# Optimization experiments

Measured on AMD Instinct MI355X. Metric: run time of the kernel, lower is better.

The kernel has to match this reference:

```python
import jax, jax.numpy as jnp
import numpy as np

B = 131072
D = 64          # d_model
T = 4           # num_tiles
TEMP = 0.5


def setup_inputs() -> dict:
    key = jax.random.key(0)
    ks = jax.random.split(key, 16)
    s = 0.02
    return {
        "a_vec": jax.random.normal(ks[0], (B, D), dtype=jnp.float32),
        "b_vec": jax.random.normal(ks[1], (B, D), dtype=jnp.float32),
        "pos_encoding": jax.random.normal(ks[2], (B, 8), dtype=jnp.float32),
        # router: Linear(2D+8 -> D), GELU, Linear(D -> T)
        "Wr1": jax.random.normal(ks[3], (2 * D + 8, D), dtype=jnp.float32) * s,
        "br1": jnp.zeros((D,), dtype=jnp.float32),
        "Wr2": jax.random.normal(ks[4], (D, T), dtype=jnp.float32) * s,
        "br2": jnp.zeros((T,), dtype=jnp.float32),
        # tile nets: per-tile Linear(2D -> 2D), GELU, Linear(2D -> D)
        "W1": jax.random.normal(ks[5], (T, 2 * D, 2 * D), dtype=jnp.float32) * s,
        "b1": jnp.zeros((T, 2 * D), dtype=jnp.float32),
        "W2": jax.random.normal(ks[6], (T, 2 * D, D), dtype=jnp.float32) * s,
        "b2": jnp.zeros((T, D), dtype=jnp.float32),
    }


def _router(x, Wr1, br1, Wr2, br2):
    h = jax.nn.gelu(x @ Wr1 + br1, approximate=False)  # torch nn.GELU is exact
    return (h @ Wr2 + br2) / TEMP


def reference(a_vec, b_vec, pos_encoding, Wr1, br1, Wr2, br2, W1, b1, W2, b2):
    pair = jnp.concatenate([a_vec, b_vec], axis=-1)            # (B, 2D)

    # Routing 1 uses pair; routing 2 uses flipped pair. Both expert passes
    # consume `pair` (faithful to the original code, which feeds pair both times).
    idx1 = jnp.argmax(_router(jnp.concatenate([pair, pos_encoding], -1),
                              Wr1, br1, Wr2, br2), axis=-1)    # (B,)
    pair_flip = jnp.concatenate([b_vec, a_vec], axis=-1)
    idx2 = jnp.argmax(_router(jnp.concatenate([pair_flip, pos_encoding], -1),
                              Wr1, br1, Wr2, br2), axis=-1)    # (B,)

    # Run all tiles on every sample (small T), then gather the routed output.
    h = jax.nn.gelu(jnp.einsum('bi,tij->btj', pair, W1) + b1, approximate=False)  # (B,T,2D)
    out_all = jnp.einsum('bth,thd->btd', h, W2) + b2                              # (B,T,D)

    out1 = jnp.take_along_axis(out_all, idx1[:, None, None], axis=1)[:, 0]
    out2 = jnp.take_along_axis(out_all, idx2[:, None, None], axis=1)[:, 0]
    return out1, out2
```

## Files before the change

kernel.cpp:

```cpp
#include <hip/hip_runtime.h>

#define B_N 131072

using bfrag_t = __attribute__((ext_vector_type(8))) short;
using acc_t   = __attribute__((ext_vector_type(4))) float;
using v4f     = __attribute__((ext_vector_type(4))) float;
using i32x4_t = __attribute__((ext_vector_type(4))) int;

__device__ __forceinline__ unsigned short f2bf(float f) {
  unsigned int u = __float_as_uint(f);
  u += 0x7FFFu + ((u >> 16) & 1u);
  return (unsigned short)(u >> 16);
}

__device__ __forceinline__ unsigned int pk2bf(float x, float y) {
  return (unsigned int)f2bf(x) | ((unsigned int)f2bf(y) << 16);
}

__device__ __forceinline__ void gload_lds16(const void* g, void* l) {
  __builtin_amdgcn_global_load_lds((const __attribute__((address_space(1))) void*)g,
                                   (__attribute__((address_space(3))) void*)l, 16, 0, 0);
}

__device__ __forceinline__ float gelu_f(float x) {
  float ax = fabsf(x) * 0.70710678118654752f;
  float t  = __builtin_amdgcn_rcpf(fmaf(0.3275911f, ax, 1.0f));
  float p  = fmaf(1.061405429f, t, -1.453152027f);
  p = fmaf(p, t, 1.421413741f);
  p = fmaf(p, t, -0.284496736f);
  p = fmaf(p, t, 0.254829592f);
  p = p * t;
  float e  = __expf(-ax * ax);
  float er = fmaf(-p, e, 1.0f);
  er = (x < 0.0f) ? -er : er;
  return 0.5f * x * (1.0f + er);
}

__global__ __launch_bounds__(256) void prepack2_k(
    const float* __restrict__ Wr1, const float* __restrict__ br1,
    const float* __restrict__ Wr2, const float* __restrict__ br2,
    const float* __restrict__ W1, const float* __restrict__ W2,
    float* __restrict__ RW, short* __restrict__ W1s, short* __restrict__ W2s,
    unsigned int* __restrict__ counts) {
  int gt = blockIdx.x * 256 + threadIdx.x;
  if (gt < 4) counts[gt] = 0u;
  for (int idx = gt; idx < 142 * 64; idx += 16384) {
    int row = idx >> 6, j = idx & 63; float val;
    if (row < 136)      val = Wr1[row * 64 + j];
    else if (row == 136) val = br1[j];
    else if (row < 141) val = Wr2[(row - 137) * 64 + j];
    else                val = (j < 4) ? br2[j] : 0.0f;
    RW[idx] = val;
  }
  for (int ch = gt; ch < 8192; ch += 16384) {
    int t = ch >> 11, r = (ch >> 4) & 127, c = ch & 15;
    const float* src = W1 + t * 16384 + r;
    short* dst = W1s + (t * 128 + r) * 128 + ((c ^ (r & 15)) * 8);
    #pragma unroll
    for (int m = 0; m < 8; m++) dst[m] = (short)f2bf(src[(c * 8 + m) * 128]);
  }
  for (int ch = gt; ch < 4096; ch += 16384) {
    int t = ch >> 10, d = (ch >> 4) & 63, c = ch & 15;
    const float* src = W2 + t * 8192 + d;
    short* dst = W2s + (t * 64 + d) * 128 + ((c ^ (d & 15)) * 8);
    #pragma unroll
    for (int m = 0; m < 8; m++) dst[m] = (short)f2bf(src[(c * 8 + m) * 64]);
  }
}

__global__ __launch_bounds__(256, 4) void router8_k(
    const float* __restrict__ a, const float* __restrict__ b,
    const float* __restrict__ pos, const float* __restrict__ RW,
    unsigned char* __restrict__ r1, unsigned char* __restrict__ r2,
    unsigned int* __restrict__ gcounts) {
  __shared__ float SB[8832];
  int tid = threadIdx.x, lane = tid & 63;
  int s0 = blockIdx.x * 64;

  #pragma unroll
  for (int it = 0; it < 8; it++) {
    int idx = it * 256 + tid;
    int s = idx >> 5, c = idx & 31;
    const float* src = (c < 16) ? (a + (size_t)(s0 + s) * 64 + c * 4)
                                : (b + (size_t)(s0 + s) * 64 + (c - 16) * 4);
    v4f v = *(const v4f*)src;
    float* dst = SB + s * 129 + c * 4;
    dst[0] = v[0]; dst[1] = v[1]; dst[2] = v[2]; dst[3] = v[3];
  }
  #pragma unroll
  for (int r = 0; r < 2; r++) {
    int idx = r * 256 + tid;
    int s = idx >> 3, c = idx & 7;
    SB[8256 + s * 9 + c] = pos[(size_t)(s0 + s) * 8 + c];
  }
  __syncthreads();

  int wch = __builtin_amdgcn_readfirstlane(tid >> 6) * 16;
  const float* Wb = RW + wch;
  float acc1[16], acc2[16];
  #pragma unroll
  for (int c = 0; c < 16; c++) {
    float bi = RW[136 * 64 + wch + c];
    acc1[c] = bi; acc2[c] = bi;
  }
  const float* Xrow = SB + lane * 129;
  #pragma unroll 2
  for (int i = 0; i < 64; i++) {
    float xa = Xrow[i];
    float xb = Xrow[64 + i];
    const float* w = Wb + i * 64;
    #pragma unroll
    for (int c = 0; c < 16; c++) {
      float wv = w[c];
      acc1[c] = fmaf(xa, wv, acc1[c]);
      acc2[c] = fmaf(xb, wv, acc2[c]);
    }
  }
  #pragma unroll 2
  for (int i = 0; i < 64; i++) {
    float xa = Xrow[i];
    float xb = Xrow[64 + i];
    const float* w = Wb + (64 + i) * 64;
    #pragma unroll
    for (int c = 0; c < 16; c++) {
      float wv = w[c];
      acc1[c] = fmaf(xb, wv, acc1[c]);
      acc2[c] = fmaf(xa, wv, acc2[c]);
    }
  }
  const float* Prow = SB + 8256 + lane * 9;
  #pragma unroll 2
  for (int i = 0; i < 8; i++) {
    float p = Prow[i];
    const float* w = Wb + (128 + i) * 64;
    #pragma unroll
    for (int c = 0; c < 16; c++) {
      float wv = w[c];
      acc1[c] = fmaf(p, wv, acc1[c]);
      acc2[c] = fmaf(p, wv, acc2[c]);
    }
  }
  #pragma unroll
  for (int c = 0; c < 16; c++) {
    acc1[c] = gelu_f(acc1[c]);
    acc2[c] = gelu_f(acc2[c]);
  }
  __syncthreads();
  #pragma unroll
  for (int c = 0; c < 16; c++) {
    SB[lane * 65 + wch + c] = acc1[c];
    SB[4160 + lane * 65 + wch + c] = acc2[c];
  }
  __syncthreads();
  float l1[4], l2[4];
  #pragma unroll
  for (int m = 0; m < 4; m++) {
    float bi = RW[141 * 64 + m];
    l1[m] = bi; l2[m] = bi;
  }
  #pragma unroll 4
  for (int j = 0; j < 64; j++) {
    float h1 = SB[lane * 65 + j];
    float h2 = SB[4160 + lane * 65 + j];
    const float* w2 = RW + 137 * 64 + j * 4;
    #pragma unroll
    for (int m = 0; m < 4; m++) {
      float wv = w2[m];
      l1[m] = fmaf(h1, wv, l1[m]);
      l2[m] = fmaf(h2, wv, l2[m]);
    }
  }
  int idx1 = 0; float b1v = l1[0];
  if (l1[1] > b1v) { b1v = l1[1]; idx1 = 1; }
  if (l1[2] > b1v) { b1v = l1[2]; idx1 = 2; }
  if (l1[3] > b1v) { b1v = l1[3]; idx1 = 3; }
  int idx2 = 0; float b2v = l2[0];
  if (l2[1] > b2v) { b2v = l2[1]; idx2 = 1; }
  if (l2[2] > b2v) { b2v = l2[2]; idx2 = 2; }
  if (l2[3] > b2v) { b2v = l2[3]; idx2 = 3; }
  if (tid < 64) {
    r1[s0 + lane] = (unsigned char)idx1;
    r2[s0 + lane] = (unsigned char)idx2;
    #pragma unroll
    for (int t = 0; t < 4; t++) {
      unsigned long long m1 = __ballot(idx1 == t);
      unsigned long long m2 = __ballot(idx2 == t);
      if (lane == 0)
        atomicAdd(gcounts + t, (unsigned int)(__popcll(m1) + __popcll(m2)));
    }
  }
}

__global__ __launch_bounds__(256) void offsets_k(
    const unsigned int* __restrict__ counts, unsigned int* __restrict__ table,
    unsigned int* __restrict__ cursors, unsigned int* __restrict__ list) {
  __shared__ unsigned int ps[5], cnt[4];
  int tid = threadIdx.x;
  if (tid == 0) {
    unsigned int acc = 0;
    for (int t = 0; t < 4; t++) {
      ps[t] = acc;
      unsigned int c = counts[t];
      cnt[t] = c;
      acc += ((c + 127u) >> 7) << 7;
    }
    ps[4] = acc;
    #pragma unroll
    for (int t = 0; t < 5; t++) table[t] = ps[t];
    #pragma unroll
    for (int t = 0; t < 4; t++) cursors[t] = ps[t];
  }
  __syncthreads();
  #pragma unroll
  for (int r = 0; r < 2; r++) {
    int idx = r * 256 + tid;
    int t = idx >> 7, i = idx & 127;
    unsigned int pos = ps[t] + cnt[t] + (unsigned int)i;
    if (pos < ps[t + 1]) list[pos] = 0xFFFFFFFFu;
  }
}

__global__ __launch_bounds__(256) void place_k(
    const unsigned char* __restrict__ r1, const unsigned char* __restrict__ r2,
    unsigned int* __restrict__ cursors, unsigned int* __restrict__ list) {
  __shared__ unsigned int lc[4], lb[4];
  int tid = threadIdx.x;
  if (tid < 4) lc[tid] = 0u;
  __syncthreads();
  int s = blockIdx.x * 256 + tid;
  int e1 = (int)r1[s], e2 = (int)r2[s];
  unsigned int k1 = atomicAdd(&lc[e1], 1u);
  unsigned int k2 = atomicAdd(&lc[e2], 1u);
  __syncthreads();
  if (tid < 4) lb[tid] = atomicAdd(&cursors[tid], lc[tid]);
  __syncthreads();
  list[lb[e1] + k1] = ((unsigned int)s << 1);
  list[lb[e2] + k2] = ((unsigned int)s << 1) | 1u;
}

__global__ __launch_bounds__(256) void expert3_k(
    const float* __restrict__ a, const float* __restrict__ b,
    const short* __restrict__ W1s, const short* __restrict__ W2s,
    const float* __restrict__ b1, const float* __restrict__ b2,
    const unsigned int* __restrict__ table, const unsigned int* __restrict__ list,
    float* __restrict__ out) {
  __shared__ short LB[24576];
  __shared__ unsigned int eLS[128];
  int tid = threadIdx.x;
  int wave = tid >> 6, lane = tid & 63;
  int q = lane >> 4, sm = lane & 15;

  unsigned int p0 = blockIdx.x * 128u;
  unsigned int t1 = table[1], t2 = table[2], t3 = table[3], t4 = table[4];
  if (p0 >= t4) return;
  int t = (p0 >= t1) + (p0 >= t2) + (p0 >= t3);

  if (tid < 128) eLS[tid] = list[p0 + tid];
  __syncthreads();

  #pragma unroll
  for (int r = 0; r < 8; r++) {
    int slot = r * 256 + tid;
    int g = slot >> 10, sg = slot & 1023;
    int f = sg >> 6, l = sg & 63;
    int sgrp = f >> 2, kb = f & 3;
    int ls2 = g * 64 + sgrp * 16 + (l & 15);
    unsigned int e = eLS[ls2];
    int s = (e == 0xFFFFFFFFu) ? 0 : (int)(e >> 1);
    int k = kb * 32 + (l >> 4) * 8;
    const float* src = (k < 64) ? (a + (size_t)s * 64 + k) : (b + (size_t)s * 64 + (k - 64));
    acc_t v0 = *(const acc_t*)(src);
    acc_t v1 = *(const acc_t*)(src + 4);
    i32x4_t pk;
    pk[0] = (int)pk2bf(v0[0], v0[1]);
    pk[1] = (int)pk2bf(v0[2], v0[3]);
    pk[2] = (int)pk2bf(v1[0], v1[1]);
    pk[3] = (int)pk2bf(v1[2], v1[3]);
    *(i32x4_t*)(&LB[slot * 8]) = pk;
  }
  __syncthreads();
  bfrag_t bfrag[2][4];
  #pragma unroll
  for (int g = 0; g < 2; g++)
    #pragma unroll
    for (int kb = 0; kb < 4; kb++)
      bfrag[g][kb] = *(const bfrag_t*)(&LB[((g * 16 + wave * 4 + kb) * 64 + lane) * 8]);

  unsigned int eA = eLS[wave * 16 + sm];
  unsigned int eB = eLS[64 + wave * 16 + sm];
  __syncthreads();

  acc_t zero = {0.f, 0.f, 0.f, 0.f};
  int vb[4];
  #pragma unroll
  for (int kb = 0; kb < 4; kb++) vb[kb] = sm * 256 + (((kb * 4 + q) ^ sm) * 16);
  int addr0 = (((q & 1) * 2) * 16 + sm) * 4;
  int addr1 = addr0 + 64;
  bool hi = (q >> 1) != 0;

  #pragma unroll
  for (int it = 0; it < 12; it++) {
    int cb = it * 256 + wave * 64;
    int chunk = cb + lane;
    const short* gsrc = (chunk < 2048) ? (W1s + t * 16384 + chunk * 8)
                                       : (W2s + t * 8192 + (chunk - 2048) * 8);
    gload_lds16(gsrc, (char*)LB + cb * 16);
  }
  __syncthreads();

  #pragma unroll
  for (int g = 0; g < 2; g++) {
    unsigned int hp[8][2];
    #pragma unroll
    for (int mt = 0; mt < 8; mt++) {
      acc_t c = zero;
      #pragma unroll
      for (int kb = 0; kb < 4; kb++) {
        bfrag_t A = *(const bfrag_t*)((const char*)LB + mt * 4096 + vb[kb]);
        c = __builtin_amdgcn_mfma_f32_16x16x32_bf16(A, bfrag[g][kb], c, 0, 0, 0);
      }
      acc_t bv = *(const acc_t*)(b1 + t * 128 + mt * 16 + q * 4);
      float g0 = gelu_f(c[0] + bv[0]);
      float g1 = gelu_f(c[1] + bv[1]);
      float g2 = gelu_f(c[2] + bv[2]);
      float g3 = gelu_f(c[3] + bv[3]);
      hp[mt][0] = pk2bf(g0, g1);
      hp[mt][1] = pk2bf(g2, g3);
    }
    bfrag_t b2f[4];
    #pragma unroll
    for (int kb2 = 0; kb2 < 4; kb2++) {
      int p00 = __builtin_amdgcn_ds_bpermute(addr0, (int)hp[2 * kb2][0]);
      int p01 = __builtin_amdgcn_ds_bpermute(addr0, (int)hp[2 * kb2][1]);
      int p10 = __builtin_amdgcn_ds_bpermute(addr1, (int)hp[2 * kb2][0]);
      int p11 = __builtin_amdgcn_ds_bpermute(addr1, (int)hp[2 * kb2][1]);
      int q00 = __builtin_amdgcn_ds_bpermute(addr0, (int)hp[2 * kb2 + 1][0]);
      int q01 = __builtin_amdgcn_ds_bpermute(addr0, (int)hp[2 * kb2 + 1][1]);
      int q10 = __builtin_amdgcn_ds_bpermute(addr1, (int)hp[2 * kb2 + 1][0]);
      int q11 = __builtin_amdgcn_ds_bpermute(addr1, (int)hp[2 * kb2 + 1][1]);
      i32x4_t w;
      w[0] = hi ? q00 : p00;
      w[1] = hi ? q01 : p01;
      w[2] = hi ? q10 : p10;
      w[3] = hi ? q11 : p11;
      b2f[kb2] = __builtin_bit_cast(bfrag_t, w);
    }
    unsigned int e = g ? eB : eA;
    bool live = (e != 0xFFFFFFFFu);
    size_t so = ((size_t)(e & 1u)) * B_N + (size_t)(e >> 1);
    float* p = out + so * 64 + q * 4;
    #pragma unroll
    for (int mt2 = 0; mt2 < 4; mt2++) {
      acc_t c = zero;
      #pragma unroll
      for (int kb2 = 0; kb2 < 4; kb2++) {
        bfrag_t A = *(const bfrag_t*)((const char*)LB + 32768 + mt2 * 4096 + vb[kb2]);
        c = __builtin_amdgcn_mfma_f32_16x16x32_bf16(A, b2f[kb2], c, 0, 0, 0);
      }
      acc_t bv = *(const acc_t*)(b2 + t * 64 + mt2 * 16 + q * 4);
      c[0] += bv[0]; c[1] += bv[1]; c[2] += bv[2]; c[3] += bv[3];
      if (live) *(acc_t*)(p + mt2 * 16) = c;
    }
  }
}

extern "C" void kernel_launch(void* const* d_in, const int* in_sizes, int n_in,
                              void* d_out, int out_size, void* d_ws, size_t ws_size,
                              hipStream_t stream) {
  const float* a   = (const float*)d_in[0];
  const float* bv  = (const float*)d_in[1];
  const float* pos = (const float*)d_in[2];
  const float* Wr1 = (const float*)d_in[3];
  const float* br1 = (const float*)d_in[4];
  const float* Wr2 = (const float*)d_in[5];
  const float* br2 = (const float*)d_in[6];
  const float* W1  = (const float*)d_in[7];
  const float* b1  = (const float*)d_in[8];
  const float* W2  = (const float*)d_in[9];
  const float* b2  = (const float*)d_in[10];
  float* out = (float*)d_out;

  unsigned char* r1 = (unsigned char*)d_ws;
  unsigned char* r2 = r1 + B_N;
  float* RW  = (float*)((char*)d_ws + 262144);
  short* W1s = (short*)((char*)d_ws + 298496);
  short* W2s = (short*)((char*)d_ws + 429568);
  unsigned int* counts  = (unsigned int*)((char*)d_ws + 495104);
  unsigned int* cursors = (unsigned int*)((char*)d_ws + 495120);
  unsigned int* table   = (unsigned int*)((char*)d_ws + 495136);
  unsigned int* list    = (unsigned int*)((char*)d_ws + 495168);

  prepack2_k<<<64, 256, 0, stream>>>(Wr1, br1, Wr2, br2, W1, W2, RW, W1s, W2s, counts);
  router8_k<<<B_N / 64, 256, 0, stream>>>(a, bv, pos, RW, r1, r2, counts);
  offsets_k<<<1, 256, 0, stream>>>(counts, table, cursors, list);
  place_k<<<B_N / 256, 256, 0, stream>>>(r1, r2, cursors, list);
  expert3_k<<<2052, 256, 0, stream>>>(a, bv, W1s, W2s, b1, b2, table, list, out);
}
```

Measured before the change: 304.3 us.

## Restructure router to hold weights in registers and use DPP argmax

The router kernel is rewritten so each lane keeps one hidden column of the first router layer (136 weights) plus a column of the second layer in registers. Each wave processes 32 samples in groups of 4, reading sample inputs through wave-uniform (broadcast) global loads instead of staging them in LDS. The 4-way argmax is done with DPP quad permutes, and routing counts are aggregated per block before one global atomic. This removes repeated weight loads and most LDS traffic, but uses many VGPRs (launch bounds drop to 2 blocks) and relies on scalar or broadcast loads of activations.

After: 1.040 ms. +241.6%, slower.

```diff
diff --git a/kernel.cpp b/kernel.cpp
--- a/kernel.cpp
+++ b/kernel.cpp
@@ -35,6 +35,9 @@
   er = (x < 0.0f) ? -er : er;
   return 0.5f * x * (1.0f + er);
 }
+
+#define QP_F(v, CTRL) __int_as_float(__builtin_amdgcn_mov_dpp(__float_as_int(v), (CTRL), 0xF, 0xF, false))
+#define QP_I(v, CTRL) __builtin_amdgcn_mov_dpp((v), (CTRL), 0xF, 0xF, false)
 
 __global__ __launch_bounds__(256) void prepack2_k(
     const float* __restrict__ Wr1, const float* __restrict__ br1,
@@ -68,127 +71,117 @@
   }
 }
 
-__global__ __launch_bounds__(256, 4) void router8_k(
+__global__ __launch_bounds__(256, 2) void router10_k(
     const float* __restrict__ a, const float* __restrict__ b,
     const float* __restrict__ pos, const float* __restrict__ RW,
     unsigned char* __restrict__ r1, unsigned char* __restrict__ r2,
     unsigned int* __restrict__ gcounts) {
-  __shared__ float SB[8832];
+  __shared__ float HX[4 * 64 * 10];
+  __shared__ unsigned int hcnt[4];
   int tid = threadIdx.x, lane = tid & 63;
-  int s0 = blockIdx.x * 64;
-
-  #pragma unroll
-  for (int it = 0; it < 8; it++) {
-    int idx = it * 256 + tid;
-    int s = idx >> 5, c = idx & 31;
-    const float* src = (c < 16) ? (a + (size_t)(s0 + s) * 64 + c * 4)
-                                : (b + (size_t)(s0 + s) * 64 + (c - 16) * 4);
-    v4f v = *(const v4f*)src;
-    float* dst = SB + s * 129 + c * 4;
-    dst[0] = v[0]; dst[1] = v[1]; dst[2] = v[2]; dst[3] = v[3];
-  }
-  #pragma unroll
-  for (int r = 0; r < 2; r++) {
-    int idx = r * 256 + tid;
-    int s = idx >> 3, c = idx & 7;
-    SB[8256 + s * 9 + c] = pos[(size_t)(s0 + s) * 8 + c];
-  }
-  __syncthreads();
-
-  int wch = __builtin_amdgcn_readfirstlane(tid >> 6) * 16;
-  const float* Wb = RW + wch;
-  float acc1[16], acc2[16];
-  #pragma unroll
-  for (int c = 0; c < 16; c++) {
-    float bi = RW[136 * 64 + wch + c];
-    acc1[c] = bi; acc2[c] = bi;
-  }
-  const float* Xrow = SB + lane * 129;
-  #pragma unroll 2
-  for (int i = 0; i < 64; i++) {
-    float xa = Xrow[i];
-    float xb = Xrow[64 + i];
-    const float* w = Wb + i * 64;
-    #pragma unroll
-    for (int c = 0; c < 16; c++) {
-      float wv = w[c];
-      acc1[c] = fmaf(xa, wv, acc1[c]);
-      acc2[c] = fmaf(xb, wv, acc2[c]);
-    }
-  }
-  #pragma unroll 2
-  for (int i = 0; i < 64; i++) {
-    float xa = Xrow[i];
-    float xb = Xrow[64 + i];
-    const float* w = Wb + (64 + i) * 64;
-    #pragma unroll
-    for (int c = 0; c < 16; c++) {
-      float wv = w[c];
-      acc1[c] = fmaf(xb, wv, acc1[c]);
-      acc2[c] = fmaf(xa, wv, acc2[c]);
-    }
-  }
-  const float* Prow = SB + 8256 + lane * 9;
-  #pragma unroll 2
-  for (int i = 0; i < 8; i++) {
-    float p = Prow[i];
-    const float* w = Wb + (128 + i) * 64;
-    #pragma unroll
-    for (int c = 0; c < 16; c++) {
-      float wv = w[c];
-      acc1[c] = fmaf(p, wv, acc1[c]);
-      acc2[c] = fmaf(p, wv, acc2[c]);
-    }
-  }
-  #pragma unroll
-  for (int c = 0; c < 16; c++) {
-    acc1[c] = gelu_f(acc1[c]);
-    acc2[c] = gelu_f(acc2[c]);
-  }
-  __syncthreads();
-  #pragma unroll
-  for (int c = 0; c < 16; c++) {
-    SB[lane * 65 + wch + c] = acc1[c];
-    SB[4160 + lane * 65 + wch + c] = acc2[c];
-  }
-  __syncthreads();
-  float l1[4], l2[4];
-  #pragma unroll
-  for (int m = 0; m < 4; m++) {
-    float bi = RW[141 * 64 + m];
-    l1[m] = bi; l2[m] = bi;
-  }
-  #pragma unroll 4
-  for (int j = 0; j < 64; j++) {
-    float h1 = SB[lane * 65 + j];
-    float h2 = SB[4160 + lane * 65 + j];
-    const float* w2 = RW + 137 * 64 + j * 4;
-    #pragma unroll
-    for (int m = 0; m < 4; m++) {
-      float wv = w2[m];
-      l1[m] = fmaf(h1, wv, l1[m]);
-      l2[m] = fmaf(h2, wv, l2[m]);
-    }
-  }
-  int idx1 = 0; float b1v = l1[0];
-  if (l1[1] > b1v) { b1v = l1[1]; idx1 = 1; }
-  if (l1[2] > b1v) { b1v = l1[2]; idx1 = 2; }
-  if (l1[3] > b1v) { b1v = l1[3]; idx1 = 3; }
-  int idx2 = 0; float b2v = l2[0];
-  if (l2[1] > b2v) { b2v = l2[1]; idx2 = 1; }
-  if (l2[2] > b2v) { b2v = l2[2]; idx2 = 2; }
-  if (l2[3] > b2v) { b2v = l2[3]; idx2 = 3; }
-  if (tid < 64) {
-    r1[s0 + lane] = (unsigned char)idx1;
-    r2[s0 + lane] = (unsigned char)idx2;
+  int wave = __builtin_amdgcn_readfirstlane(tid >> 6);
+  if (tid < 4) hcnt[tid] = 0u;
+  __syncthreads();
+
+  float Wreg[136];
+  #pragma unroll
+  for (int i = 0; i < 136; i++) Wreg[i] = RW[i * 64 + lane];
+  float br1v = RW[136 * 64 + lane];
+  int m = lane & 3, s_of = (lane >> 2) & 3;
+  float w2col[64];
+  #pragma unroll
+  for (int j = 0; j < 64; j++) w2col[j] = RW[137 * 64 + j * 4 + m];
+  float br2v = RW[141 * 64 + m];
+
+  unsigned int c1[4] = {0u, 0u, 0u, 0u}, c2[4] = {0u, 0u, 0u, 0u};
+  int wgid = blockIdx.x * 4 + wave;
+  int sbase = wgid * 32;
+  bool voter = (lane < 16) && (m == 0);
+
+  #pragma unroll 1
+  for (int g = 0; g < 8; g++) {
+    int s0g = sbase + g * 4;
+    float acc1[4], acc2[4];
+    #pragma unroll
+    for (int s = 0; s < 4; s++) { acc1[s] = br1v; acc2[s] = br1v; }
+    #pragma unroll
+    for (int i = 0; i < 64; i++) {
+      #pragma unroll
+      for (int s = 0; s < 4; s++) {
+        float xa = a[(size_t)(s0g + s) * 64 + i];
+        float xb = b[(size_t)(s0g + s) * 64 + i];
+        acc1[s] = fmaf(xa, Wreg[i], acc1[s]);
+        acc2[s] = fmaf(xb, Wreg[i], acc2[s]);
+      }
+    }
+    #pragma unroll
+    for (int i = 0; i < 64; i++) {
+      #pragma unroll
+      for (int s = 0; s < 4; s++) {
+        float xa = a[(size_t)(s0g + s) * 64 + i];
+        float xb = b[(size_t)(s0g + s) * 64 + i];
+        acc1[s] = fmaf(xb, Wreg[64 + i], acc1[s]);
+        acc2[s] = fmaf(xa, Wreg[64 + i], acc2[s]);
+      }
+    }
+    #pragma unroll
+    for (int i = 0; i < 8; i++) {
+      #pragma unroll
+      for (int s = 0; s < 4; s++) {
+        float p = pos[(size_t)(s0g + s) * 8 + i];
+        acc1[s] = fmaf(p, Wreg[128 + i], acc1[s]);
+        acc2[s] = fmaf(p, Wreg[128 + i], acc2[s]);
+      }
+    }
+    #pragma unroll
+    for (int s = 0; s < 4; s++) {
+      float h1 = gelu_f(acc1[s]);
+      float h2 = gelu_f(acc2[s]);
+      float2* dst = (float2*)&HX[(wave * 64 + lane) * 10 + s * 2];
+      *dst = float2{h1, h2};
+    }
+    float l1 = br2v, l2 = br2v;
+    #pragma unroll 8
+    for (int j = 0; j < 64; j++) {
+      float2 h = *(const float2*)&HX[(wave * 64 + j) * 10 + s_of * 2];
+      l1 = fmaf(h.x, w2col[j], l1);
+      l2 = fmaf(h.y, w2col[j], l2);
+    }
+    float o1 = QP_F(l1, 0xB1), o2 = QP_F(l2, 0xB1);
+    bool odd = (m & 1) != 0;
+    float vhi1 = odd ? l1 : o1, vlo1 = odd ? o1 : l1;
+    float vhi2 = odd ? l2 : o2, vlo2 = odd ? o2 : l2;
+    int ihi = m | 1, ilo = m & ~1;
+    bool w1 = vhi1 > vlo1, w2_ = vhi2 > vlo2;
+    float bv1 = w1 ? vhi1 : vlo1;  int bi1 = w1 ? ihi : ilo;
+    float bv2 = w2_ ? vhi2 : vlo2; int bi2 = w2_ ? ihi : ilo;
+    float p1 = QP_F(bv1, 0x4E); int q1 = QP_I(bi1, 0x4E);
+    float p2 = QP_F(bv2, 0x4E); int q2 = QP_I(bi2, 0x4E);
+    bool hi2 = (m & 2) != 0;
+    float uhi1 = hi2 ? bv1 : p1, ulo1 = hi2 ? p1 : bv1;
+    int   jhi1 = hi2 ? bi1 : q1, jlo1 = hi2 ? q1 : bi1;
+    float uhi2 = hi2 ? bv2 : p2, ulo2 = hi2 ? p2 : bv2;
+    int   jhi2 = hi2 ? bi2 : q2, jlo2 = hi2 ? q2 : bi2;
+    int idx1 = (uhi1 > ulo1) ? jhi1 : jlo1;
+    int idx2 = (uhi2 > ulo2) ? jhi2 : jlo2;
+    if (voter) {
+      r1[s0g + (lane >> 2)] = (unsigned char)idx1;
+      r2[s0g + (lane >> 2)] = (unsigned char)idx2;
+    }
     #pragma unroll
     for (int t = 0; t < 4; t++) {
-      unsigned long long m1 = __ballot(idx1 == t);
-      unsigned long long m2 = __ballot(idx2 == t);
-      if (lane == 0)
-        atomicAdd(gcounts + t, (unsigned int)(__popcll(m1) + __popcll(m2)));
-    }
-  }
+      unsigned long long b1m = __ballot(voter && (idx1 == t));
+      unsigned long long b2m = __ballot(voter && (idx2 == t));
+      c1[t] += (unsigned int)__popcll(b1m);
+      c2[t] += (unsigned int)__popcll(b2m);
+    }
+  }
+  if (lane == 0) {
+    #pragma unroll
+    for (int t = 0; t < 4; t++) atomicAdd(&hcnt[t], c1[t] + c2[t]);
+  }
+  __syncthreads();
+  if (tid < 4) atomicAdd(gcounts + tid, hcnt[tid]);
 }
 
 __global__ __launch_bounds__(256) void offsets_k(
@@ -391,7 +384,7 @@
   unsigned int* list    = (unsigned int*)((char*)d_ws + 495168);
 
   prepack2_k<<<64, 256, 0, stream>>>(Wr1, br1, Wr2, br2, W1, W2, RW, W1s, W2s, counts);
-  router8_k<<<B_N / 64, 256, 0, stream>>>(a, bv, pos, RW, r1, r2, counts);
+  router10_k<<<1024, 256, 0, stream>>>(a, bv, pos, RW, r1, r2, counts);
   offsets_k<<<1, 256, 0, stream>>>(counts, table, cursors, list);
   place_k<<<B_N / 256, 256, 0, stream>>>(r1, r2, cursors, list);
   expert3_k<<<2052, 256, 0, stream>>>(a, bv, W1s, W2s, b1, b2, table, list, out);
```
